# Performance work log

Measured on AMD Instinct MI355X. Metric: run time of the kernel, lower is better.

The kernel has to match this reference:

```python
import jax, jax.numpy as jnp
import numpy as np

# ---- static config (matches init_kwargs) ----
N_NODES = 100_000; N_GRAPHS = 100; NPG = 1000; GRID = 32  # ceil(sqrt(1000))
N_EDGES = 1_600_000
IN_DIM = 64; POS_DIM = 16; HID = 16; HEADS = 4; HD = HID * HEADS  # 64
OUT_DIM = 10; DIV_WEIGHT = 0.1; BN_EPS = 1e-5; NEG_SLOPE = 0.2


def _segment_softmax(e, dst, n):
    emax = jax.ops.segment_max(e, dst, num_segments=n)
    p = jnp.exp(e - emax[dst])
    denom = jax.ops.segment_sum(p, dst, num_segments=n)
    return p / (denom[dst] + 1e-16)


def _gat(x, src, dst, n, W, a_src, a_dst, extra=None):
    """GATv1-style conv: per-head linear, additive attention, segment softmax over dst."""
    H, D = a_src.shape
    h = (x @ W).reshape(n, H, D)          # [N,H,D]
    s = (h * a_src).sum(-1)               # [N,H]
    d = (h * a_dst).sum(-1)               # [N,H]
    e = s[src] + d[dst]
    if extra is not None:
        e = e + extra                     # positional attention bias [E,H]
    e = jax.nn.leaky_relu(e, NEG_SLOPE)
    alpha = _segment_softmax(e, dst, n)   # [E,H]
    out = jax.ops.segment_sum(alpha[:, :, None] * h[src], dst, num_segments=n)
    return out.reshape(n, H * D)


def _div_loss(W):
    # head-diversity / orthogonality regularizer on per-head weight slices
    in_dim = W.shape[0]
    Wh = W.reshape(in_dim, HEADS, HID).transpose(1, 0, 2).reshape(HEADS, -1)
    Wn = Wh / (jnp.linalg.norm(Wh, axis=-1, keepdims=True) + 1e-12)
    G = Wn @ Wn.T
    off = G - jnp.eye(HEADS, dtype=W.dtype)
    return DIV_WEIGHT * (off ** 2).sum() / (HEADS * (HEADS - 1))


def _grid_pos(n, dtype):
    # normalized grid positions per graph (equal-size graphs of NPG nodes)
    i = jnp.arange(n) % NPG
    return jnp.stack([(i // GRID) / (GRID - 1), (i % GRID) / (GRID - 1)], -1).astype(dtype)


def _forward(x, edge_index, batch,
             pe_W, pe_b,
             l0_pW, l0_pas, l0_pad, l0_posW, l0_posb, l0_dW, l0_das, l0_dad, l0_fW, l0_fb, l0_g, l0_b,
             l1_pW, l1_pas, l1_pad, l1_posW, l1_posb, l1_dW, l1_das, l1_dad, l1_fW, l1_fb, l1_g, l1_b,
             res_W, res_b, task_W, task_b):
    n = x.shape[0]
    src, dst = edge_index[0], edge_index[1]
    pos = _grid_pos(n, x.dtype)
    rel = pos[dst] - pos[src]             # [E,2]
    h = jnp.concatenate([x, pos @ pe_W + pe_b], -1)  # positional encoding concat [N,80]

    def layer(h_in, pW, pas, pad, posW, posb, dW, das, dad, fW, fb, g, b):
        pos_out = _gat(h_in, src, dst, n, pW, pas, pad, extra=rel @ posW + posb)
        div_out = _gat(h_in, src, dst, n, dW, das, dad)
        fused = jnp.concatenate([pos_out, div_out], -1) @ fW + fb
        mu = fused.mean(0)
        var = fused.var(0)
        bn = (fused - mu) / jnp.sqrt(var + BN_EPS) * g + b
        return jax.nn.elu(bn), _div_loss(dW)

    h1, dl0 = layer(h, l0_pW, l0_pas, l0_pad, l0_posW, l0_posb, l0_dW, l0_das, l0_dad, l0_fW, l0_fb, l0_g, l0_b)
    h2, dl1 = layer(h1, l1_pW, l1_pas, l1_pad, l1_posW, l1_posb, l1_dW, l1_das, l1_dad, l1_fW, l1_fb, l1_g, l1_b)
    h2 = h2 + (h1 @ res_W + res_b)        # residual on layer >0

    pooled = jax.ops.segment_sum(h2, batch, num_segments=N_GRAPHS) / NPG  # mean pool
    task = pooled @ task_W + task_b       # [N_GRAPHS, OUT_DIM]
    return task, dl0 + dl1


def setup_inputs() -> dict:
    key = jax.random.key(0)
    keys = iter(jax.random.split(key, 64))
    nk = lambda: next(keys)
    w = lambda shape: jax.random.normal(nk(), shape, jnp.float32) * 0.05
    x = jax.random.normal(nk(), (N_NODES, IN_DIM), jnp.float32)
    gid = jnp.repeat(jnp.arange(N_GRAPHS), N_EDGES // N_GRAPHS)
    src = gid * NPG + jax.random.randint(nk(), (N_EDGES,), 0, NPG)
    dst = gid * NPG + jax.random.randint(nk(), (N_EDGES,), 0, NPG)
    edge_index = jnp.stack([src, dst]).astype(jnp.int32)
    batch = jnp.repeat(jnp.arange(N_GRAPHS), NPG).astype(jnp.int32)
    IN0 = IN_DIM + POS_DIM
    inp = dict(x=x, edge_index=edge_index, batch=batch,
               pe_W=w((2, POS_DIM)), pe_b=jnp.zeros((POS_DIM,), jnp.float32))
    for pref, din in (('l0', IN0), ('l1', HD)):
        inp[pref + '_pW'] = w((din, HD)); inp[pref + '_pas'] = w((HEADS, HID)); inp[pref + '_pad'] = w((HEADS, HID))
        inp[pref + '_posW'] = w((2, HEADS)); inp[pref + '_posb'] = jnp.zeros((HEADS,), jnp.float32)
        inp[pref + '_dW'] = w((din, HD)); inp[pref + '_das'] = w((HEADS, HID)); inp[pref + '_dad'] = w((HEADS, HID))
        inp[pref + '_fW'] = w((2 * HD, HD)); inp[pref + '_fb'] = jnp.zeros((HD,), jnp.float32)
        inp[pref + '_g'] = jnp.ones((HD,), jnp.float32); inp[pref + '_b'] = jnp.zeros((HD,), jnp.float32)
    inp['res_W'] = w((HD, HD)); inp['res_b'] = jnp.zeros((HD,), jnp.float32)
    inp['task_W'] = w((HD, OUT_DIM)); inp['task_b'] = jnp.zeros((OUT_DIM,), jnp.float32)
    return inp


def reference(x, edge_index, batch,
              pe_W, pe_b,
              l0_pW, l0_pas, l0_pad, l0_posW, l0_posb, l0_dW, l0_das, l0_dad, l0_fW, l0_fb, l0_g, l0_b,
              l1_pW, l1_pas, l1_pad, l1_posW, l1_posb, l1_dW, l1_das, l1_dad, l1_fW, l1_fb, l1_g, l1_b,
              res_W, res_b, task_W, task_b):
    return _forward(x, edge_index, batch, pe_W, pe_b,
                    l0_pW, l0_pas, l0_pad, l0_posW, l0_posb, l0_dW, l0_das, l0_dad, l0_fW, l0_fb, l0_g, l0_b,
                    l1_pW, l1_pas, l1_pad, l1_posW, l1_posb, l1_dW, l1_das, l1_dad, l1_fW, l1_fb, l1_g, l1_b,
                    res_W, res_b, task_W, task_b)
```

## Files before the change

### kernel.cpp

```cpp
#include <hip/hip_runtime.h>
#include <math.h>

#define N_NODES   100000
#define N_GRAPHS  100
#define NPG       1000
#define N_EDGES   1600000
#define EPG       16000
#define HID       16
#define HEADS     4
#define HD        64
#define OUT_DIM   10
#define BN_EPS    1e-5f
#define NEG_SLOPE 0.2f

#define LDA 68

static const size_t OFF_PEWS  = 7000000;
static const size_t OFF_WFRAG = 7010000;
static const size_t OFF_WF2   = 7020000;
static const size_t OFF_POOL  = 7100000;
static const size_t OFF_HL    = 8000000;
static const size_t OFF_CAT   = 20800000;
static const size_t OFF_F0    = 33600000;
static const size_t OFF_F1    = 40000000;
static const size_t OFF_SPS   = 46400000;
static const size_t OFF_DPD   = 47200000;
static const size_t OFF_STATS = 48000000;
static const size_t OFF_CSR   = 48000128;
static const size_t OFF_SRT   = 48100144;

__device__ inline unsigned bf_pack(float x, float y) {
    unsigned ux = __float_as_uint(x);
    unsigned uy = __float_as_uint(y);
    ux = (ux + 0x7FFFu + ((ux >> 16) & 1u)) >> 16;
    uy = ((uy + 0x7FFFu + ((uy >> 16) & 1u)) >> 16) << 16;
    return ux | uy;
}
__device__ inline float bf_lo(unsigned u) { return __uint_as_float(u << 16); }
__device__ inline float bf_hi(unsigned u) { return __uint_as_float(u & 0xFFFF0000u); }

typedef __attribute__((ext_vector_type(8))) short bf16x8;
typedef __attribute__((ext_vector_type(4))) float f32x4;

__device__ inline bf16x8 frag_from(unsigned a, unsigned b, unsigned c, unsigned d) {
    uint4 u{a, b, c, d};
    return *reinterpret_cast<bf16x8*>(&u);
}

__global__ __launch_bounds__(1024) void sort_edges(const int* __restrict__ ei,
                                                   int* __restrict__ csr_off,
                                                   int* __restrict__ sorted_src) {
    __shared__ int hist[1024];
    __shared__ int scan[1024];
    const int g = blockIdx.x;
    const int t = threadIdx.x;
    const int* src = ei;
    const int* dst = ei + N_EDGES;
    const int e0 = g * EPG;
    const int nbase = g * NPG;

    hist[t] = 0;
    __syncthreads();
    for (int i = t; i < EPG; i += 1024) {
        int d = dst[e0 + i] - nbase;
        atomicAdd(&hist[d], 1);
    }
    __syncthreads();
    scan[t] = hist[t];
    __syncthreads();
    for (int off = 1; off < 1024; off <<= 1) {
        int v = (t >= off) ? scan[t - off] : 0;
        __syncthreads();
        scan[t] += v;
        __syncthreads();
    }
    int excl = scan[t] - hist[t];
    if (t < NPG) csr_off[nbase + t] = e0 + excl;
    if (g == 0 && t == 0) csr_off[N_NODES] = N_EDGES;
    __syncthreads();
    hist[t] = excl;
    __syncthreads();
    for (int i = t; i < EPG; i += 1024) {
        int s = src[e0 + i];
        int d = dst[e0 + i] - nbase;
        int slot = atomicAdd(&hist[d], 1);
        sorted_src[e0 + slot] = s;
    }
}

__global__ void prep_pe(const float* __restrict__ peW, const float* __restrict__ peb,
                        const float* __restrict__ Wp, const float* __restrict__ Wd,
                        float* __restrict__ pe) {
    int t = threadIdx.x;
    if (t < 128) {
        int r = t >> 6, c = t & 63;
        float sp = 0.f, sd = 0.f;
        for (int m = 0; m < 16; ++m) {
            sp += peW[r * 16 + m] * Wp[(64 + m) * 64 + c];
            sd += peW[r * 16 + m] * Wd[(64 + m) * 64 + c];
        }
        pe[r * 64 + c] = sp;
        pe[192 + r * 64 + c] = sd;
    } else if (t < 192) {
        int c = t & 63;
        float sp = 0.f, sd = 0.f;
        for (int m = 0; m < 16; ++m) {
            sp += peb[m] * Wp[(64 + m) * 64 + c];
            sd += peb[m] * Wd[(64 + m) * 64 + c];
        }
        pe[128 + c] = sp;
        pe[320 + c] = sd;
    }
}

__global__ void prep_wfrag(const float* __restrict__ fW0, const float* __restrict__ fW1,
                           uint4* __restrict__ wf) {
    const int t = threadIdx.x;
    for (int i = t; i < 2 * 4 * 4 * 64; i += 256) {
        const int lane  = i & 63;
        const int ct    = (i >> 6) & 3;
        const int kk    = (i >> 8) & 3;
        const int layer = i >> 10;
        const float* W = layer ? fW1 : fW0;
        const int col = ct * 16 + (lane & 15);
        const int kb  = kk * 32 + (lane >> 4) * 8;
        uint4 u;
        u.x = bf_pack(W[(kb + 0) * 64 + col], W[(kb + 1) * 64 + col]);
        u.y = bf_pack(W[(kb + 2) * 64 + col], W[(kb + 3) * 64 + col]);
        u.z = bf_pack(W[(kb + 4) * 64 + col], W[(kb + 5) * 64 + col]);
        u.w = bf_pack(W[(kb + 6) * 64 + col], W[(kb + 7) * 64 + col]);
        wf[i] = u;
    }
}

__global__ void prep_wfrag_dual(const float* __restrict__ pW0, const float* __restrict__ dW0,
                                const float* __restrict__ pW1, const float* __restrict__ dW1,
                                uint4* __restrict__ wf) {
    const int t = threadIdx.x;
    for (int i = t; i < 2048; i += 256) {
        const int lane  = i & 63;
        const int ct    = (i >> 6) & 3;
        const int kk    = (i >> 8) & 1;
        const int mat   = (i >> 9) & 1;
        const int layer = i >> 10;
        const float* W = layer ? (mat ? dW1 : pW1) : (mat ? dW0 : pW0);
        const int col = ct * 16 + (lane & 15);
        const int kb  = kk * 32 + (lane >> 4) * 8;
        uint4 u;
        u.x = bf_pack(W[(kb + 0) * 64 + col], W[(kb + 1) * 64 + col]);
        u.y = bf_pack(W[(kb + 2) * 64 + col], W[(kb + 3) * 64 + col]);
        u.z = bf_pack(W[(kb + 4) * 64 + col], W[(kb + 5) * 64 + col]);
        u.w = bf_pack(W[(kb + 6) * 64 + col], W[(kb + 7) * 64 + col]);
        wf[i] = u;
    }
}

template <bool PE>
__global__ __launch_bounds__(256) void gemm_dual_mfma(const float* __restrict__ A,
                                                      const unsigned* __restrict__ wf2,
                                                      const float* __restrict__ pe,
                                                      const float* __restrict__ pas,
                                                      const float* __restrict__ pad_,
                                                      const float* __restrict__ das,
                                                      const float* __restrict__ dad,
                                                      const float* __restrict__ posW,
                                                      const float* __restrict__ posb,
                                                      unsigned* __restrict__ hl,
                                                      float2* __restrict__ sps,
                                                      float2* __restrict__ dpd) {
    __shared__ float sD[4 * 2 * 16 * LDA];
    const int t = threadIdx.x;
    const int w = t >> 6, lane = t & 63;
    const int cidx = lane & 15, khi = lane >> 4;
    const int node0 = blockIdx.x * 64;

    bf16x8 wf[2][2][4];
#pragma unroll
    for (int mat = 0; mat < 2; ++mat)
#pragma unroll
        for (int kk = 0; kk < 2; ++kk)
#pragma unroll
            for (int ct = 0; ct < 4; ++ct)
                wf[mat][kk][ct] = *reinterpret_cast<const bf16x8*>(
                    wf2 + (size_t)((((mat * 2 + kk) * 4 + ct) * 64) + lane) * 4);

    int gn = node0 + w * 16 + cidx; if (gn > N_NODES - 1) gn = N_NODES - 1;
    const float* ar = A + (size_t)gn * 64;
    bf16x8 ah[2], al[2];
#pragma unroll
    for (int kk = 0; kk < 2; ++kk) {
        const int k0 = kk * 32 + khi * 8;
        float4 f0 = *reinterpret_cast<const float4*>(ar + k0);
        float4 f1 = *reinterpret_cast<const float4*>(ar + k0 + 4);
        unsigned h0 = bf_pack(f0.x, f0.y), h1 = bf_pack(f0.z, f0.w);
        unsigned h2 = bf_pack(f1.x, f1.y), h3 = bf_pack(f1.z, f1.w);
        unsigned l0 = bf_pack(f0.x - bf_lo(h0), f0.y - bf_hi(h0));
        unsigned l1 = bf_pack(f0.z - bf_lo(h1), f0.w - bf_hi(h1));
        unsigned l2 = bf_pack(f1.x - bf_lo(h2), f1.y - bf_hi(h2));
        unsigned l3 = bf_pack(f1.z - bf_lo(h3), f1.w - bf_hi(h3));
        ah[kk] = frag_from(h0, h1, h2, h3);
        al[kk] = frag_from(l0, l1, l2, l3);
    }

    f32x4 ap[4], ad[4];
#pragma unroll
    for (int ct = 0; ct < 4; ++ct) { ap[ct] = 0.f; ad[ct] = 0.f; }
#pragma unroll
    for (int ct = 0; ct < 4; ++ct) {
        ap[ct] = __builtin_amdgcn_mfma_f32_16x16x32_bf16(ah[0], wf[0][0][ct], ap[ct], 0, 0, 0);
        ap[ct] = __builtin_amdgcn_mfma_f32_16x16x32_bf16(ah[1], wf[0][1][ct], ap[ct], 0, 0, 0);
        ap[ct] = __builtin_amdgcn_mfma_f32_16x16x32_bf16(al[0], wf[0][0][ct], ap[ct], 0, 0, 0);
        ap[ct] = __builtin_amdgcn_mfma_f32_16x16x32_bf16(al[1], wf[0][1][ct], ap[ct], 0, 0, 0);
        ad[ct] = __builtin_amdgcn_mfma_f32_16x16x32_bf16(ah[0], wf[1][0][ct], ad[ct], 0, 0, 0);
        ad[ct] = __builtin_amdgcn_mfma_f32_16x16x32_bf16(ah[1], wf[1][1][ct], ad[ct], 0, 0, 0);
        ad[ct] = __builtin_amdgcn_mfma_f32_16x16x32_bf16(al[0], wf[1][0][ct], ad[ct], 0, 0, 0);
        ad[ct] = __builtin_amdgcn_mfma_f32_16x16x32_bf16(al[1], wf[1][1][ct], ad[ct], 0, 0, 0);
    }

    {
        float* base = sD + w * (2 * 16 * LDA);
#pragma unroll
        for (int ct = 0; ct < 4; ++ct)
#pragma unroll
            for (int q = 0; q < 4; ++q) {
                base[(khi * 4 + q) * LDA + ct * 16 + cidx]                 = ap[ct][q];
                base[16 * LDA + (khi * 4 + q) * LDA + ct * 16 + cidx]      = ad[ct][q];
            }
    }
    __syncthreads();

    const int tx = t & 15, ty = t >> 4;
    const int c4 = tx * 4;
    float4 accp[4], accd[4];
#pragma unroll
    for (int j = 0; j < 4; ++j) {
        const int n = ty * 4 + j;
        const float* bp = sD + (n >> 4) * (2 * 16 * LDA) + (n & 15) * LDA;
        accp[j] = *reinterpret_cast<const float4*>(bp + c4);
        accd[j] = *reinterpret_cast<const float4*>(bp + 16 * LDA + c4);
    }

    if (PE) {
        float4 pp0 = *reinterpret_cast<const float4*>(&pe[c4]);
        float4 pp1 = *reinterpret_cast<const float4*>(&pe[64 + c4]);
        float4 ppb = *reinterpret_cast<const float4*>(&pe[128 + c4]);
        float4 pd0 = *reinterpret_cast<const float4*>(&pe[192 + c4]);
        float4 pd1 = *reinterpret_cast<const float4*>(&pe[256 + c4]);
        float4 pdb = *reinterpret_cast<const float4*>(&pe[320 + c4]);
#pragma unroll
        for (int j = 0; j < 4; ++j) {
            int node = node0 + ty * 4 + j;
            int r = node % NPG;
            float px = (float)(r >> 5) * (1.0f / 31.0f);
            float py = (float)(r & 31) * (1.0f / 31.0f);
            accp[j].x += px * pp0.x + py * pp1.x + ppb.x;
            accp[j].y += px * pp0.y + py * pp1.y + ppb.y;
            accp[j].z += px * pp0.z + py * pp1.z + ppb.z;
            accp[j].w += px * pp0.w + py * pp1.w + ppb.w;
            accd[j].x += px * pd0.x + py * pd1.x + pdb.x;
            accd[j].y += px * pd0.y + py * pd1.y + pdb.y;
            accd[j].z += px * pd0.z + py * pd1.z + pdb.z;
            accd[j].w += px * pd0.w + py * pd1.w + pdb.w;
        }
    }

    float4 pasv = *reinterpret_cast<const float4*>(&pas[c4]);
    float4 padv = *reinterpret_cast<const float4*>(&pad_[c4]);
    float4 dasv = *reinterpret_cast<const float4*>(&das[c4]);
    float4 dadv = *reinterpret_cast<const float4*>(&dad[c4]);
    const int h = tx >> 2;
    const float pw0 = posW[h], pw1 = posW[4 + h], pb = posb[h];
    const int cu = tx * 2;
#pragma unroll
    for (int j = 0; j < 4; ++j) {
        const int node = node0 + ty * 4 + j;
        float vps = accp[j].x * pasv.x + accp[j].y * pasv.y + accp[j].z * pasv.z + accp[j].w * pasv.w;
        float vpd = accp[j].x * padv.x + accp[j].y * padv.y + accp[j].z * padv.z + accp[j].w * padv.w;
        float vds = accd[j].x * dasv.x + accd[j].y * dasv.y + accd[j].z * dasv.z + accd[j].w * dasv.w;
        float vdd = accd[j].x * dadv.x + accd[j].y * dadv.y + accd[j].z * dadv.z + accd[j].w * dadv.w;
        vps += __shfl_xor(vps, 1); vps += __shfl_xor(vps, 2);
        vpd += __shfl_xor(vpd, 1); vpd += __shfl_xor(vpd, 2);
        vds += __shfl_xor(vds, 1); vds += __shfl_xor(vds, 2);
        vdd += __shfl_xor(vdd, 1); vdd += __shfl_xor(vdd, 2);
        if (node < N_NODES) {
            uint2 up, ud;
            up.x = bf_pack(accp[j].x, accp[j].y); up.y = bf_pack(accp[j].z, accp[j].w);
            ud.x = bf_pack(accd[j].x, accd[j].y); ud.y = bf_pack(accd[j].z, accd[j].w);
            *reinterpret_cast<uint2*>(&hl[(size_t)node * 64 + cu])      = up;
            *reinterpret_cast<uint2*>(&hl[(size_t)node * 64 + 32 + cu]) = ud;
            if ((tx & 3) == 0) {
                const int r = node % NPG;
                const float pxn = (float)(r >> 5) * (1.0f / 31.0f);
                const float pyn = (float)(r & 31) * (1.0f / 31.0f);
                const float posdot = pxn * pw0 + pyn * pw1;
                sps[node * 4 + h] = float2{vps - posdot, vds};
                dpd[node * 4 + h] = float2{vpd + posdot + pb, vdd};
            }
        }
    }
}

__global__ __launch_bounds__(256) void gemm_mfma_bf(const unsigned* __restrict__ A,
                                                    const unsigned* __restrict__ wfrag,
                                                    const float* __restrict__ bias,
                                                    float* __restrict__ out,
                                                    float* __restrict__ stats) {
    __shared__ float red[512];
    const int t = threadIdx.x;
    const int lane = t & 63;
    const int cidx = lane & 15;
    const int khi  = lane >> 4;

    bf16x8 wf[4][4];
#pragma unroll
    for (int kk = 0; kk < 4; ++kk)
#pragma unroll
        for (int ct = 0; ct < 4; ++ct)
            wf[kk][ct] = *reinterpret_cast<const bf16x8*>(wfrag + (size_t)((kk * 4 + ct) * 64 + lane) * 4);

    float bias_r[4];
#pragma unroll
    for (int ct = 0; ct < 4; ++ct) bias_r[ct] = bias[ct * 16 + cidx];

    float ls[4] = {0.f, 0.f, 0.f, 0.f};
    float lq[4] = {0.f, 0.f, 0.f, 0.f};

    const int NW  = gridDim.x << 2;
    const int wid = (blockIdx.x << 2) + (t >> 6);
    for (int tile = wid; tile < N_NODES / 16; tile += NW) {
        const int node0 = tile << 4;
        const unsigned* arow = A + (size_t)(node0 + cidx) * 64 + khi * 4;
        bf16x8 a0 = *reinterpret_cast<const bf16x8*>(arow);
        bf16x8 a1 = *reinterpret_cast<const bf16x8*>(arow + 16);
        bf16x8 a2 = *reinterpret_cast<const bf16x8*>(arow + 32);
        bf16x8 a3 = *reinterpret_cast<const bf16x8*>(arow + 48);

        f32x4 acc[4];
#pragma unroll
        for (int ct = 0; ct < 4; ++ct) acc[ct] = 0.f;
#pragma unroll
        for (int ct = 0; ct < 4; ++ct) {
            acc[ct] = __builtin_amdgcn_mfma_f32_16x16x32_bf16(a0, wf[0][ct], acc[ct], 0, 0, 0);
            acc[ct] = __builtin_amdgcn_mfma_f32_16x16x32_bf16(a1, wf[1][ct], acc[ct], 0, 0, 0);
            acc[ct] = __builtin_amdgcn_mfma_f32_16x16x32_bf16(a2, wf[2][ct], acc[ct], 0, 0, 0);
            acc[ct] = __builtin_amdgcn_mfma_f32_16x16x32_bf16(a3, wf[3][ct], acc[ct], 0, 0, 0);
        }

        const int nbase = node0 + (khi << 2);
#pragma unroll
        for (int ct = 0; ct < 4; ++ct) {
#pragma unroll
            for (int q = 0; q < 4; ++q) {
                float v = acc[ct][q] + bias_r[ct];
                out[(size_t)(nbase + q) * 64 + ct * 16 + cidx] = v;
                ls[ct] += v;
                lq[ct] = fmaf(v, v, lq[ct]);
            }
        }
    }

#pragma unroll
    for (int ct = 0; ct < 4; ++ct) {
        ls[ct] += __shfl_xor(ls[ct], 16); ls[ct] += __shfl_xor(ls[ct], 32);
        lq[ct] += __shfl_xor(lq[ct], 16); lq[ct] += __shfl_xor(lq[ct], 32);
    }
    if (lane < 16) {
        const int w = t >> 6;
#pragma unroll
        for (int ct = 0; ct < 4; ++ct) {
            red[w * 64 + ct * 16 + lane]       = ls[ct];
            red[256 + w * 64 + ct * 16 + lane] = lq[ct];
        }
    }
    __syncthreads();
    if (t < 64) {
        float s  = red[t] + red[64 + t] + red[128 + t] + red[192 + t];
        float sq = red[256 + t] + red[320 + t] + red[384 + t] + red[448 + t];
        atomicAdd(&stats[t], s);
        atomicAdd(&stats[64 + t], sq);
    }
}

__global__ __launch_bounds__(256) void gat_fused(const unsigned* __restrict__ hl,
                                                 const float2* __restrict__ sps,
                                                 const float2* __restrict__ dpd,
                                                 const int* __restrict__ csr_off,
                                                 const int* __restrict__ sorted_src,
                                                 unsigned* __restrict__ gat_cat) {
    const int b = blockIdx.x;
    const int logical = (b & 7) * 3125 + (b >> 3);
    const int v = logical * 4 + (threadIdx.x >> 6);
    if (v >= N_NODES) return;
    const int lane = threadIdx.x & 63;
    const int j1 = lane >> 3;
    const int p1 = (lane >> 2) & 1;
    const int h1 = lane & 3;
    const int phneed = ((lane >> 5) << 2) | ((lane & 31) >> 3);

    const float2 dv1 = dpd[(size_t)v * 4 + h1];
    const float dval1 = p1 ? dv1.y : dv1.x;

    const int beg = __builtin_amdgcn_readfirstlane(csr_off[v]);
    const int end = __builtin_amdgcn_readfirstlane(csr_off[v + 1]);

    float2 acc = {0.f, 0.f};
    float wpart = 0.f;
    int e = beg;
    for (; e + 8 <= end; e += 8) {
        int s = sorted_src[e + j1];
        float2 sv = sps[(size_t)s * 4 + h1];
        float elog = (p1 ? sv.y : sv.x) + dval1;
        elog = fmaxf(elog, NEG_SLOPE * elog);
        float w = __expf(elog);
        wpart += w;
#pragma unroll
        for (int jj = 0; jj < 8; ++jj) {
            int sj = __builtin_amdgcn_readlane(s, jj * 8);
            float wj = __shfl(w, jj * 8 + phneed);
            unsigned u = hl[((size_t)sj << 6) + lane];
            acc.x = fmaf(wj, bf_lo(u), acc.x);
            acc.y = fmaf(wj, bf_hi(u), acc.y);
        }
    }
    if (e < end) {
        const int nj = end - e;
        int ee = e + j1; if (ee >= end) ee = end - 1;
        int s = sorted_src[ee];
        float2 sv = sps[(size_t)s * 4 + h1];
        float elog = (p1 ? sv.y : sv.x) + dval1;
        elog = fmaxf(elog, NEG_SLOPE * elog);
        float w = __expf(elog);
        if (j1 >= nj) w = 0.f;
        wpart += w;
        for (int jj = 0; jj < nj; ++jj) {
            int sj = __builtin_amdgcn_readlane(s, jj * 8);
            float wj = __shfl(w, jj * 8 + phneed);
            unsigned u = hl[((size_t)sj << 6) + lane];
            acc.x = fmaf(wj, bf_lo(u), acc.x);
            acc.y = fmaf(wj, bf_hi(u), acc.y);
        }
    }
    wpart += __shfl_xor(wpart, 8);
    wpart += __shfl_xor(wpart, 16);
    wpart += __shfl_xor(wpart, 32);
    const float wsum = __shfl(wpart, phneed);
    const float inv = 1.0f / (wsum + 1e-16f);
    gat_cat[(size_t)v * 64 + lane] = bf_pack(acc.x * inv, acc.y * inv);
}

template <bool WRITEF>
__global__ __launch_bounds__(256) void bn_elu(float* __restrict__ F, const float* __restrict__ stats,
                                              const float* __restrict__ gamma, const float* __restrict__ beta,
                                              float* __restrict__ pooled) {
    __shared__ float red[256];
    const int t = threadIdx.x;
    const int idx = blockIdx.x * 256 + t;
    const int c = t & 63;
    float mu = stats[c] * (1.0f / (float)N_NODES);
    float var = stats[64 + c] * (1.0f / (float)N_NODES) - mu * mu;
    float inv = rsqrtf(var + BN_EPS);
    float v = (F[idx] - mu) * inv * gamma[c] + beta[c];
    v = (v > 0.f) ? v : expm1f(v);
    if (WRITEF) F[idx] = v;
    red[t] = v;
    __syncthreads();
    if (t < 64) {
        float s = red[c] + red[64 + c] + red[128 + c] + red[192 + c];
        int g = (blockIdx.x * 4) / NPG;
        atomicAdd(&pooled[g * 64 + c], s);
    }
}

__global__ __launch_bounds__(64) void task_head(const float* __restrict__ pooled,
                                                const float* __restrict__ pooledF0,
                                                const float* __restrict__ resW,
                                                const float* __restrict__ resb,
                                                const float* __restrict__ taskW,
                                                const float* __restrict__ taskb,
                                                float* __restrict__ out) {
    const int g = blockIdx.x;
    const int c = threadIdx.x;
    float rc = 0.f;
    const float* pf = pooledF0 + g * 64;
    for (int k = 0; k < 64; ++k)
        rc = fmaf(pf[k], resW[k * 64 + c], rc);
    float p = (pooled[g * 64 + c] + rc) * (1.0f / (float)NPG) + resb[c];
#pragma unroll
    for (int o = 0; o < OUT_DIM; ++o) {
        float partial = p * taskW[c * OUT_DIM + o];
#pragma unroll
        for (int m = 1; m < 64; m <<= 1) partial += __shfl_xor(partial, m);
        if (c == 0) out[g * OUT_DIM + o] = partial + taskb[o];
    }
}

__global__ __launch_bounds__(256) void div_loss(const float* __restrict__ dW0,
                                                const float* __restrict__ dW1,
                                                float* __restrict__ out) {
    __shared__ float red[16][16];
    float total = 0.f;
    for (int layer = 0; layer < 2; ++layer) {
        const float* W = layer ? dW1 : dW0;
        const int din = layer ? 64 : 80;
        const int p = threadIdx.x & 15;
        const int s16 = threadIdx.x >> 4;
        const int i = p >> 2, j = p & 3;
        float acc = 0.f;
        const int Kk = din * 16;
        for (int kk = s16; kk < Kk; kk += 16) {
            int rrow = kk >> 4, cc = kk & 15;
            acc += W[rrow * 64 + i * 16 + cc] * W[rrow * 64 + j * 16 + cc];
        }
        red[p][s16] = acc;
        __syncthreads();
        if (threadIdx.x < 16) {
            float s = 0.f;
            for (int m = 0; m < 16; ++m) s += red[threadIdx.x][m];
            red[threadIdx.x][0] = s;
        }
        __syncthreads();
        if (threadIdx.x == 0) {
            float G[4][4], nrm[4];
            for (int a = 0; a < 4; ++a)
                for (int b = 0; b < 4; ++b) G[a][b] = red[a * 4 + b][0];
            for (int a = 0; a < 4; ++a) nrm[a] = sqrtf(G[a][a]) + 1e-12f;
            float l = 0.f;
            for (int a = 0; a < 4; ++a)
                for (int b = 0; b < 4; ++b) {
                    float gn = G[a][b] / (nrm[a] * nrm[b]);
                    float off = gn - (a == b ? 1.f : 0.f);
                    l += off * off;
                }
            total += 0.1f * l / 12.f;
        }
        __syncthreads();
    }
    if (threadIdx.x == 0) *out = total;
}

extern "C" void kernel_launch(void* const* d_in, const int* in_sizes, int n_in,
                              void* d_out, int out_size, void* d_ws, size_t ws_size,
                              hipStream_t stream) {
    const float* x      = (const float*)d_in[0];
    const int*   ei     = (const int*)d_in[1];
    const float* peW    = (const float*)d_in[3];
    const float* peb    = (const float*)d_in[4];

    const float* l_pW[2]   = {(const float*)d_in[5],  (const float*)d_in[17]};
    const float* l_pas[2]  = {(const float*)d_in[6],  (const float*)d_in[18]};
    const float* l_pad[2]  = {(const float*)d_in[7],  (const float*)d_in[19]};
    const float* l_posW[2] = {(const float*)d_in[8],  (const float*)d_in[20]};
    const float* l_posb[2] = {(const float*)d_in[9],  (const float*)d_in[21]};
    const float* l_dW[2]   = {(const float*)d_in[10], (const float*)d_in[22]};
    const float* l_das[2]  = {(const float*)d_in[11], (const float*)d_in[23]};
    const float* l_dad[2]  = {(const float*)d_in[12], (const float*)d_in[24]};
    const float* l_fW[2]   = {(const float*)d_in[13], (const float*)d_in[25]};
    const float* l_fb[2]   = {(const float*)d_in[14], (const float*)d_in[26]};
    const float* l_g[2]    = {(const float*)d_in[15], (const float*)d_in[27]};
    const float* l_b[2]    = {(const float*)d_in[16], (const float*)d_in[28]};
    const float* res_W  = (const float*)d_in[29];
    const float* res_b  = (const float*)d_in[30];
    const float* task_W = (const float*)d_in[31];
    const float* task_b = (const float*)d_in[32];

    float* ws = (float*)d_ws;
    float* pe_ws   = ws + OFF_PEWS;
    float* wfrag   = ws + OFF_WFRAG;
    float* wfrag2  = ws + OFF_WF2;
    float* pooled  = ws + OFF_POOL;
    float* pooledF0= ws + OFF_POOL + 6400;
    unsigned* hl   = (unsigned*)(ws + OFF_HL);
    unsigned* cat_bf = (unsigned*)(ws + OFF_CAT);
    float* F0      = ws + OFF_F0;
    float* F1      = ws + OFF_F1;
    float2* sps    = (float2*)(ws + OFF_SPS);
    float2* dpd    = (float2*)(ws + OFF_DPD);
    float* stats   = ws + OFF_STATS;
    int*   csr_off    = (int*)(ws + OFF_CSR);
    int*   sorted_src = (int*)(ws + OFF_SRT);
    float* out = (float*)d_out;

    const int NODE_BLOCKS = (N_NODES + 3) / 4;
    const int GEMM_BLOCKS = (N_NODES + 63) / 64;
    const int MFMA_BLOCKS = 1563;
    const int BN_BLOCKS   = N_NODES * 64 / 256;

    sort_edges<<<N_GRAPHS, 1024, 0, stream>>>(ei, csr_off, sorted_src);
    prep_pe<<<1, 256, 0, stream>>>(peW, peb, l_pW[0], l_dW[0], pe_ws);
    prep_wfrag<<<1, 256, 0, stream>>>(l_fW[0], l_fW[1], (uint4*)wfrag);
    prep_wfrag_dual<<<1, 256, 0, stream>>>(l_pW[0], l_dW[0], l_pW[1], l_dW[1], (uint4*)wfrag2);
    hipMemsetAsync(pooled, 0, 2 * N_GRAPHS * 64 * sizeof(float), stream);

    gemm_dual_mfma<true><<<GEMM_BLOCKS, 256, 0, stream>>>(x, (const unsigned*)wfrag2, pe_ws,
        l_pas[0], l_pad[0], l_das[0], l_dad[0], l_posW[0], l_posb[0],
        hl, sps, dpd);
    gat_fused<<<NODE_BLOCKS, 256, 0, stream>>>(hl, sps, dpd, csr_off, sorted_src, cat_bf);
    hipMemsetAsync(stats, 0, 128 * sizeof(float), stream);
    gemm_mfma_bf<<<MFMA_BLOCKS, 256, 0, stream>>>(cat_bf, (const unsigned*)wfrag,
                                                  l_fb[0], F0, stats);
    bn_elu<true><<<BN_BLOCKS, 256, 0, stream>>>(F0, stats, l_g[0], l_b[0], pooledF0);

    gemm_dual_mfma<false><<<GEMM_BLOCKS, 256, 0, stream>>>(F0, (const unsigned*)wfrag2 + 4096, pe_ws,
        l_pas[1], l_pad[1], l_das[1], l_dad[1], l_posW[1], l_posb[1],
        hl, sps, dpd);
    gat_fused<<<NODE_BLOCKS, 256, 0, stream>>>(hl, sps, dpd, csr_off, sorted_src, cat_bf);
    hipMemsetAsync(stats, 0, 128 * sizeof(float), stream);
    gemm_mfma_bf<<<MFMA_BLOCKS, 256, 0, stream>>>(cat_bf, (const unsigned*)wfrag + 4096,
                                                  l_fb[1], F1, stats);
    bn_elu<false><<<BN_BLOCKS, 256, 0, stream>>>(F1, stats, l_g[1], l_b[1], pooled);

    task_head<<<N_GRAPHS, 64, 0, stream>>>(pooled, pooledF0, res_W, res_b,
                                           task_W, task_b, out);
    div_loss<<<1, 256, 0, stream>>>(l_dW[0], l_dW[1], out + 1000);
}
```

Measured before the change: 483.1 us.

## Fuse layer-0 BN+ELU into layer-1 GEMM, merge prep kernels, prefetch GAT sources

Removes the layer-0 bn_elu pass by applying batch-norm scale/shift and ELU while loading F0 inside the layer-1 dual GEMM, which also does the per-graph pooling with wave shuffles and atomics. The three prep kernels and the memsets are merged into one 4-block prep_all launch, and the two layers now use separate stats buffers. The source-score array is split into two planar float arrays, and the GAT edge loop software-pipelines the sorted_src and score loads two iterations ahead. The cost is extra per-element BN/ELU arithmetic and atomics in the GEMM, plus more registers held in the GAT loop.

After: 496.3 us. 2.7% more time.

```diff
diff --git a/kernel.cpp b/kernel.cpp
--- a/kernel.cpp
+++ b/kernel.cpp
@@ -16,6 +16,7 @@
 #define LDA 68
 
 static const size_t OFF_PEWS  = 7000000;
+static const size_t OFF_STAT1 = 7001000;
 static const size_t OFF_WFRAG = 7010000;
 static const size_t OFF_WF2   = 7020000;
 static const size_t OFF_POOL  = 7100000;
@@ -23,7 +24,8 @@
 static const size_t OFF_CAT   = 20800000;
 static const size_t OFF_F0    = 33600000;
 static const size_t OFF_F1    = 40000000;
-static const size_t OFF_SPS   = 46400000;
+static const size_t OFF_SPSP  = 46400000;
+static const size_t OFF_SPSD  = 46800000;
 static const size_t OFF_DPD   = 47200000;
 static const size_t OFF_STATS = 48000000;
 static const size_t OFF_CSR   = 48000128;
@@ -88,74 +90,78 @@
     }
 }
 
-__global__ void prep_pe(const float* __restrict__ peW, const float* __restrict__ peb,
-                        const float* __restrict__ Wp, const float* __restrict__ Wd,
-                        float* __restrict__ pe) {
-    int t = threadIdx.x;
-    if (t < 128) {
-        int r = t >> 6, c = t & 63;
-        float sp = 0.f, sd = 0.f;
-        for (int m = 0; m < 16; ++m) {
-            sp += peW[r * 16 + m] * Wp[(64 + m) * 64 + c];
-            sd += peW[r * 16 + m] * Wd[(64 + m) * 64 + c];
-        }
-        pe[r * 64 + c] = sp;
-        pe[192 + r * 64 + c] = sd;
-    } else if (t < 192) {
-        int c = t & 63;
-        float sp = 0.f, sd = 0.f;
-        for (int m = 0; m < 16; ++m) {
-            sp += peb[m] * Wp[(64 + m) * 64 + c];
-            sd += peb[m] * Wd[(64 + m) * 64 + c];
-        }
-        pe[128 + c] = sp;
-        pe[320 + c] = sd;
-    }
-}
-
-__global__ void prep_wfrag(const float* __restrict__ fW0, const float* __restrict__ fW1,
-                           uint4* __restrict__ wf) {
+__global__ __launch_bounds__(256) void prep_all(const float* __restrict__ peW, const float* __restrict__ peb,
+                                                const float* __restrict__ pW0, const float* __restrict__ dW0,
+                                                const float* __restrict__ pW1, const float* __restrict__ dW1,
+                                                const float* __restrict__ fW0, const float* __restrict__ fW1,
+                                                float* __restrict__ pe,
+                                                uint4* __restrict__ wfA,
+                                                uint4* __restrict__ wfD,
+                                                float* __restrict__ pool2,
+                                                float* __restrict__ stats0,
+                                                float* __restrict__ stats1) {
     const int t = threadIdx.x;
-    for (int i = t; i < 2 * 4 * 4 * 64; i += 256) {
-        const int lane  = i & 63;
-        const int ct    = (i >> 6) & 3;
-        const int kk    = (i >> 8) & 3;
-        const int layer = i >> 10;
-        const float* W = layer ? fW1 : fW0;
-        const int col = ct * 16 + (lane & 15);
-        const int kb  = kk * 32 + (lane >> 4) * 8;
-        uint4 u;
-        u.x = bf_pack(W[(kb + 0) * 64 + col], W[(kb + 1) * 64 + col]);
-        u.y = bf_pack(W[(kb + 2) * 64 + col], W[(kb + 3) * 64 + col]);
-        u.z = bf_pack(W[(kb + 4) * 64 + col], W[(kb + 5) * 64 + col]);
-        u.w = bf_pack(W[(kb + 6) * 64 + col], W[(kb + 7) * 64 + col]);
-        wf[i] = u;
-    }
-}
-
-__global__ void prep_wfrag_dual(const float* __restrict__ pW0, const float* __restrict__ dW0,
-                                const float* __restrict__ pW1, const float* __restrict__ dW1,
-                                uint4* __restrict__ wf) {
-    const int t = threadIdx.x;
-    for (int i = t; i < 2048; i += 256) {
-        const int lane  = i & 63;
-        const int ct    = (i >> 6) & 3;
-        const int kk    = (i >> 8) & 1;
-        const int mat   = (i >> 9) & 1;
-        const int layer = i >> 10;
-        const float* W = layer ? (mat ? dW1 : pW1) : (mat ? dW0 : pW0);
-        const int col = ct * 16 + (lane & 15);
-        const int kb  = kk * 32 + (lane >> 4) * 8;
-        uint4 u;
-        u.x = bf_pack(W[(kb + 0) * 64 + col], W[(kb + 1) * 64 + col]);
-        u.y = bf_pack(W[(kb + 2) * 64 + col], W[(kb + 3) * 64 + col]);
-        u.z = bf_pack(W[(kb + 4) * 64 + col], W[(kb + 5) * 64 + col]);
-        u.w = bf_pack(W[(kb + 6) * 64 + col], W[(kb + 7) * 64 + col]);
-        wf[i] = u;
-    }
-}
-
-template <bool PE>
+    const int b = blockIdx.x;
+    if (b == 0) {
+        if (t < 128) {
+            int r = t >> 6, c = t & 63;
+            float sp = 0.f, sd = 0.f;
+            for (int m = 0; m < 16; ++m) {
+                sp += peW[r * 16 + m] * pW0[(64 + m) * 64 + c];
+                sd += peW[r * 16 + m] * dW0[(64 + m) * 64 + c];
+            }
+            pe[r * 64 + c] = sp;
+            pe[192 + r * 64 + c] = sd;
+        } else if (t < 192) {
+            int c = t & 63;
+            float sp = 0.f, sd = 0.f;
+            for (int m = 0; m < 16; ++m) {
+                sp += peb[m] * pW0[(64 + m) * 64 + c];
+                sd += peb[m] * dW0[(64 + m) * 64 + c];
+            }
+            pe[128 + c] = sp;
+            pe[320 + c] = sd;
+        }
+    } else if (b == 1) {
+        for (int i = t; i < 2 * 4 * 4 * 64; i += 256) {
+            const int lane  = i & 63;
+            const int ct    = (i >> 6) & 3;
+            const int kk    = (i >> 8) & 3;
+            const int layer = i >> 10;
+            const float* W = layer ? fW1 : fW0;
+            const int col = ct * 16 + (lane & 15);
+            const int kb  = kk * 32 + (lane >> 4) * 8;
+            uint4 u;
+            u.x = bf_pack(W[(kb + 0) * 64 + col], W[(kb + 1) * 64 + col]);
+            u.y = bf_pack(W[(kb + 2) * 64 + col], W[(kb + 3) * 64 + col]);
+            u.z = bf_pack(W[(kb + 4) * 64 + col], W[(kb + 5) * 64 + col]);
+            u.w = bf_pack(W[(kb + 6) * 64 + col], W[(kb + 7) * 64 + col]);
+            wfA[i] = u;
+        }
+    } else if (b == 2) {
+        for (int i = t; i < 2048; i += 256) {
+            const int lane  = i & 63;
+            const int ct    = (i >> 6) & 3;
+            const int kk    = (i >> 8) & 1;
+            const int mat   = (i >> 9) & 1;
+            const int layer = i >> 10;
+            const float* W = layer ? (mat ? dW1 : pW1) : (mat ? dW0 : pW0);
+            const int col = ct * 16 + (lane & 15);
+            const int kb  = kk * 32 + (lane >> 4) * 8;
+            uint4 u;
+            u.x = bf_pack(W[(kb + 0) * 64 + col], W[(kb + 1) * 64 + col]);
+            u.y = bf_pack(W[(kb + 2) * 64 + col], W[(kb + 3) * 64 + col]);
+            u.z = bf_pack(W[(kb + 4) * 64 + col], W[(kb + 5) * 64 + col]);
+            u.w = bf_pack(W[(kb + 6) * 64 + col], W[(kb + 7) * 64 + col]);
+            wfD[i] = u;
+        }
+    } else {
+        for (int i = t; i < 2 * N_GRAPHS * 64; i += 256) pool2[i] = 0.f;
+        if (t < 128) { stats0[t] = 0.f; stats1[t] = 0.f; }
+    }
+}
+
+template <bool PE, bool BN>
 __global__ __launch_bounds__(256) void gemm_dual_mfma(const float* __restrict__ A,
                                                       const unsigned* __restrict__ wf2,
                                                       const float* __restrict__ pe,
@@ -165,8 +171,13 @@
                                                       const float* __restrict__ dad,
                                                       const float* __restrict__ posW,
                                                       const float* __restrict__ posb,
+                                                      const float* __restrict__ stats,
+                                                      const float* __restrict__ gamma,
+                                                      const float* __restrict__ beta,
+                                                      float* __restrict__ poolF,
                                                       unsigned* __restrict__ hl,
-                                                      float2* __restrict__ sps,
+                                                      float* __restrict__ sps_p,
+                                                      float* __restrict__ sps_d,
                                                       float2* __restrict__ dpd) {
     __shared__ float sD[4 * 2 * 16 * LDA];
     const int t = threadIdx.x;
@@ -184,7 +195,8 @@
                 wf[mat][kk][ct] = *reinterpret_cast<const bf16x8*>(
                     wf2 + (size_t)((((mat * 2 + kk) * 4 + ct) * 64) + lane) * 4);
 
-    int gn = node0 + w * 16 + cidx; if (gn > N_NODES - 1) gn = N_NODES - 1;
+    const int node0w = node0 + w * 16;
+    int gn = node0w + cidx; if (gn > N_NODES - 1) gn = N_NODES - 1;
     const float* ar = A + (size_t)gn * 64;
     bf16x8 ah[2], al[2];
 #pragma unroll
@@ -192,6 +204,65 @@
         const int k0 = kk * 32 + khi * 8;
         float4 f0 = *reinterpret_cast<const float4*>(ar + k0);
         float4 f1 = *reinterpret_cast<const float4*>(ar + k0 + 4);
+        if (BN) {
+            const float invN = 1.0f / (float)N_NODES;
+            float4 sa = *reinterpret_cast<const float4*>(&stats[k0]);
+            float4 sb = *reinterpret_cast<const float4*>(&stats[k0 + 4]);
+            float4 qa = *reinterpret_cast<const float4*>(&stats[64 + k0]);
+            float4 qb = *reinterpret_cast<const float4*>(&stats[64 + k0 + 4]);
+            float4 ga = *reinterpret_cast<const float4*>(&gamma[k0]);
+            float4 gb = *reinterpret_cast<const float4*>(&gamma[k0 + 4]);
+            float4 ba = *reinterpret_cast<const float4*>(&beta[k0]);
+            float4 bb = *reinterpret_cast<const float4*>(&beta[k0 + 4]);
+            float sc[8], sh[8];
+            float ss[8] = {sa.x, sa.y, sa.z, sa.w, sb.x, sb.y, sb.z, sb.w};
+            float qq[8] = {qa.x, qa.y, qa.z, qa.w, qb.x, qb.y, qb.z, qb.w};
+            float gg[8] = {ga.x, ga.y, ga.z, ga.w, gb.x, gb.y, gb.z, gb.w};
+            float bt[8] = {ba.x, ba.y, ba.z, ba.w, bb.x, bb.y, bb.z, bb.w};
+#pragma unroll
+            for (int i = 0; i < 8; ++i) {
+                float mu = ss[i] * invN;
+                float var = qq[i] * invN - mu * mu;
+                float iv = rsqrtf(var + BN_EPS);
+                sc[i] = iv * gg[i];
+                sh[i] = bt[i] - mu * sc[i];
+            }
+            auto ap = [&](float v, int i) {
+                float r = fmaf(v, sc[i], sh[i]);
+                return r > 0.f ? r : (__expf(r) - 1.f);
+            };
+            f0.x = ap(f0.x, 0); f0.y = ap(f0.y, 1); f0.z = ap(f0.z, 2); f0.w = ap(f0.w, 3);
+            f1.x = ap(f1.x, 4); f1.y = ap(f1.y, 5); f1.z = ap(f1.z, 6); f1.w = ap(f1.w, 7);
+            if (node0w < N_NODES) {
+                const int node_l = node0w + cidx;
+                const bool okn = node_l < N_NODES;
+                const int gl = node_l / NPG;
+                const int g0 = node0w / NPG;
+                int lastn = node0w + 15; if (lastn > N_NODES - 1) lastn = N_NODES - 1;
+                const int g1 = lastn / NPG;
+                float p8[8] = {f0.x, f0.y, f0.z, f0.w, f1.x, f1.y, f1.z, f1.w};
+                {
+                    const bool m = okn && (gl == g0);
+#pragma unroll
+                    for (int i = 0; i < 8; ++i) {
+                        float tv = m ? p8[i] : 0.f;
+                        tv += __shfl_xor(tv, 1); tv += __shfl_xor(tv, 2);
+                        tv += __shfl_xor(tv, 4); tv += __shfl_xor(tv, 8);
+                        if (cidx == 0) atomicAdd(&poolF[g0 * 64 + k0 + i], tv);
+                    }
+                }
+                if (g1 != g0) {
+                    const bool m = okn && (gl == g1);
+#pragma unroll
+                    for (int i = 0; i < 8; ++i) {
+                        float tv = m ? p8[i] : 0.f;
+                        tv += __shfl_xor(tv, 1); tv += __shfl_xor(tv, 2);
+                        tv += __shfl_xor(tv, 4); tv += __shfl_xor(tv, 8);
+                        if (cidx == 0) atomicAdd(&poolF[g1 * 64 + k0 + i], tv);
+                    }
+                }
+            }
+        }
         unsigned h0 = bf_pack(f0.x, f0.y), h1 = bf_pack(f0.z, f0.w);
         unsigned h2 = bf_pack(f1.x, f1.y), h3 = bf_pack(f1.z, f1.w);
         unsigned l0 = bf_pack(f0.x - bf_lo(h0), f0.y - bf_hi(h0));
@@ -202,19 +273,19 @@
         al[kk] = frag_from(l0, l1, l2, l3);
     }
 
-    f32x4 ap[4], ad[4];
-#pragma unroll
-    for (int ct = 0; ct < 4; ++ct) { ap[ct] = 0.f; ad[ct] = 0.f; }
+    f32x4 ap4[4], ad4[4];
+#pragma unroll
+    for (int ct = 0; ct < 4; ++ct) { ap4[ct] = 0.f; ad4[ct] = 0.f; }
 #pragma unroll
     for (int ct = 0; ct < 4; ++ct) {
-        ap[ct] = __builtin_amdgcn_mfma_f32_16x16x32_bf16(ah[0], wf[0][0][ct], ap[ct], 0, 0, 0);
-        ap[ct] = __builtin_amdgcn_mfma_f32_16x16x32_bf16(ah[1], wf[0][1][ct], ap[ct], 0, 0, 0);
-        ap[ct] = __builtin_amdgcn_mfma_f32_16x16x32_bf16(al[0], wf[0][0][ct], ap[ct], 0, 0, 0);
-        ap[ct] = __builtin_amdgcn_mfma_f32_16x16x32_bf16(al[1], wf[0][1][ct], ap[ct], 0, 0, 0);
-        ad[ct] = __builtin_amdgcn_mfma_f32_16x16x32_bf16(ah[0], wf[1][0][ct], ad[ct], 0, 0, 0);
-        ad[ct] = __builtin_amdgcn_mfma_f32_16x16x32_bf16(ah[1], wf[1][1][ct], ad[ct], 0, 0, 0);
-        ad[ct] = __builtin_amdgcn_mfma_f32_16x16x32_bf16(al[0], wf[1][0][ct], ad[ct], 0, 0, 0);
-        ad[ct] = __builtin_amdgcn_mfma_f32_16x16x32_bf16(al[1], wf[1][1][ct], ad[ct], 0, 0, 0);
+        ap4[ct] = __builtin_amdgcn_mfma_f32_16x16x32_bf16(ah[0], wf[0][0][ct], ap4[ct], 0, 0, 0);
+        ap4[ct] = __builtin_amdgcn_mfma_f32_16x16x32_bf16(ah[1], wf[0][1][ct], ap4[ct], 0, 0, 0);
+        ap4[ct] = __builtin_amdgcn_mfma_f32_16x16x32_bf16(al[0], wf[0][0][ct], ap4[ct], 0, 0, 0);
+        ap4[ct] = __builtin_amdgcn_mfma_f32_16x16x32_bf16(al[1], wf[0][1][ct], ap4[ct], 0, 0, 0);
+        ad4[ct] = __builtin_amdgcn_mfma_f32_16x16x32_bf16(ah[0], wf[1][0][ct], ad4[ct], 0, 0, 0);
+        ad4[ct] = __builtin_amdgcn_mfma_f32_16x16x32_bf16(ah[1], wf[1][1][ct], ad4[ct], 0, 0, 0);
+        ad4[ct] = __builtin_amdgcn_mfma_f32_16x16x32_bf16(al[0], wf[1][0][ct], ad4[ct], 0, 0, 0);
+        ad4[ct] = __builtin_amdgcn_mfma_f32_16x16x32_bf16(al[1], wf[1][1][ct], ad4[ct], 0, 0, 0);
     }
 
     {
@@ -223,8 +294,8 @@
         for (int ct = 0; ct < 4; ++ct)
 #pragma unroll
             for (int q = 0; q < 4; ++q) {
-                base[(khi * 4 + q) * LDA + ct * 16 + cidx]                 = ap[ct][q];
-                base[16 * LDA + (khi * 4 + q) * LDA + ct * 16 + cidx]      = ad[ct][q];
+                base[(khi * 4 + q) * LDA + ct * 16 + cidx]                 = ap4[ct][q];
+                base[16 * LDA + (khi * 4 + q) * LDA + ct * 16 + cidx]      = ad4[ct][q];
             }
     }
     __syncthreads();
@@ -293,7 +364,8 @@
                 const float pxn = (float)(r >> 5) * (1.0f / 31.0f);
                 const float pyn = (float)(r & 31) * (1.0f / 31.0f);
                 const float posdot = pxn * pw0 + pyn * pw1;
-                sps[node * 4 + h] = float2{vps - posdot, vds};
+                sps_p[node * 4 + h] = vps - posdot;
+                sps_d[node * 4 + h] = vds;
                 dpd[node * 4 + h] = float2{vpd + posdot + pb, vdd};
             }
         }
@@ -382,7 +454,8 @@
 }
 
 __global__ __launch_bounds__(256) void gat_fused(const unsigned* __restrict__ hl,
-                                                 const float2* __restrict__ sps,
+                                                 const float* __restrict__ sps_p,
+                                                 const float* __restrict__ sps_d,
                                                  const float2* __restrict__ dpd,
                                                  const int* __restrict__ csr_off,
                                                  const int* __restrict__ sorted_src,
@@ -397,6 +470,7 @@
     const int h1 = lane & 3;
     const int phneed = ((lane >> 5) << 2) | ((lane & 31) >> 3);
 
+    const float* __restrict__ spl = p1 ? sps_d : sps_p;
     const float2 dv1 = dpd[(size_t)v * 4 + h1];
     const float dval1 = p1 ? dv1.y : dv1.x;
 
@@ -406,28 +480,38 @@
     float2 acc = {0.f, 0.f};
     float wpart = 0.f;
     int e = beg;
-    for (; e + 8 <= end; e += 8) {
-        int s = sorted_src[e + j1];
-        float2 sv = sps[(size_t)s * 4 + h1];
-        float elog = (p1 ? sv.y : sv.x) + dval1;
+    const int nfull = (end - beg) >> 3;
+
+    int sA = 0, sB = 0;
+    float svA = 0.f, svB = 0.f;
+    if (nfull >= 1) { sA = sorted_src[e + j1]; svA = spl[(size_t)sA * 4 + h1]; }
+    if (nfull >= 2) { sB = sorted_src[e + 8 + j1]; }
+
+    for (int k = 0; k < nfull; ++k, e += 8) {
+        int sC = 0;
+        if (k + 2 < nfull) sC = sorted_src[e + 16 + j1];
+        if (k + 1 < nfull) svB = spl[(size_t)sB * 4 + h1];
+        float elog = svA + dval1;
         elog = fmaxf(elog, NEG_SLOPE * elog);
         float w = __expf(elog);
         wpart += w;
 #pragma unroll
         for (int jj = 0; jj < 8; ++jj) {
-            int sj = __builtin_amdgcn_readlane(s, jj * 8);
+            int sj = __builtin_amdgcn_readlane(sA, jj * 8);
             float wj = __shfl(w, jj * 8 + phneed);
             unsigned u = hl[((size_t)sj << 6) + lane];
             acc.x = fmaf(wj, bf_lo(u), acc.x);
             acc.y = fmaf(wj, bf_hi(u), acc.y);
         }
-    }
+        sA = sB; sB = sC; svA = svB;
+    }
+
     if (e < end) {
         const int nj = end - e;
         int ee = e + j1; if (ee >= end) ee = end - 1;
         int s = sorted_src[ee];
-        float2 sv = sps[(size_t)s * 4 + h1];
-        float elog = (p1 ? sv.y : sv.x) + dval1;
+        float sval = spl[(size_t)s * 4 + h1];
+        float elog = sval + dval1;
         elog = fmaxf(elog, NEG_SLOPE * elog);
         float w = __expf(elog);
         if (j1 >= nj) w = 0.f;
@@ -565,6 +649,7 @@
 
     float* ws = (float*)d_ws;
     float* pe_ws   = ws + OFF_PEWS;
+    float* stats1  = ws + OFF_STAT1;
     float* wfrag   = ws + OFF_WFRAG;
     float* wfrag2  = ws + OFF_WF2;
     float* pooled  = ws + OFF_POOL;
@@ -573,9 +658,10 @@
     unsigned* cat_bf = (unsigned*)(ws + OFF_CAT);
     float* F0      = ws + OFF_F0;
     float* F1      = ws + OFF_F1;
-    float2* sps    = (float2*)(ws + OFF_SPS);
+    float* sps_p   = ws + OFF_SPSP;
+    float* sps_d   = ws + OFF_SPSD;
     float2* dpd    = (float2*)(ws + OFF_DPD);
-    float* stats   = ws + OFF_STATS;
+    float* stats0  = ws + OFF_STATS;
     int*   csr_off    = (int*)(ws + OFF_CSR);
     int*   sorted_src = (int*)(ws + OFF_SRT);
     float* out = (float*)d_out;
@@ -586,28 +672,27 @@
     const int BN_BLOCKS   = N_NODES * 64 / 256;
 
     sort_edges<<<N_GRAPHS, 1024, 0, stream>>>(ei, csr_off, sorted_src);
-    prep_pe<<<1, 256, 0, stream>>>(peW, peb, l_pW[0], l_dW[0], pe_ws);
-    prep_wfrag<<<1, 256, 0, stream>>>(l_fW[0], l_fW[1], (uint4*)wfrag);
-    prep_wfrag_dual<<<1, 256, 0, stream>>>(l_pW[0], l_dW[0], l_pW[1], l_dW[1], (uint4*)wfrag2);
-    hipMemsetAsync(pooled, 0, 2 * N_GRAPHS * 64 * sizeof(float), stream);
-
-    gemm_dual_mfma<true><<<GEMM_BLOCKS, 256, 0, stream>>>(x, (const unsigned*)wfrag2, pe_ws,
+    prep_all<<<4, 256, 0, stream>>>(peW, peb, l_pW[0], l_dW[0], l_pW[1], l_dW[1],
+                                    l_fW[0], l_fW[1], pe_ws,
+                                    (uint4*)wfrag, (uint4*)wfrag2,
+                                    pooled, stats0, stats1);
+
+    gemm_dual_mfma<true, false><<<GEMM_BLOCKS, 256, 0, stream>>>(x, (const unsigned*)wfrag2, pe_ws,
         l_pas[0], l_pad[0], l_das[0], l_dad[0], l_posW[0], l_posb[0],
-        hl, sps, dpd);
-    gat_fused<<<NODE_BLOCKS, 256, 0, stream>>>(hl, sps, dpd, csr_off, sorted_src, cat_bf);
-    hipMemsetAsync(stats, 0, 128 * sizeof(float), stream);
+        stats0, l_g[0], l_b[0], pooledF0,
+        hl, sps_p, sps_d, dpd);
+    gat_fused<<<NODE_BLOCKS, 256, 0, stream>>>(hl, sps_p, sps_d, dpd, csr_off, sorted_src, cat_bf);
     gemm_mfma_bf<<<MFMA_BLOCKS, 256, 0, stream>>>(cat_bf, (const unsigned*)wfrag,
-                                                  l_fb[0], F0, stats);
-    bn_elu<true><<<BN_BLOCKS, 256, 0, stream>>>(F0, stats, l_g[0], l_b[0], pooledF0);
-
-    gemm_dual_mfma<false><<<GEMM_BLOCKS, 256, 0, stream>>>(F0, (const unsigned*)wfrag2 + 4096, pe_ws,
+                                                  l_fb[0], F0, stats0);
+
+    gemm_dual_mfma<false, true><<<GEMM_BLOCKS, 256, 0, stream>>>(F0, (const unsigned*)wfrag2 + 4096, pe_ws,
         l_pas[1], l_pad[1], l_das[1], l_dad[1], l_posW[1], l_posb[1],
-        hl, sps, dpd);
-    gat_fused<<<NODE_BLOCKS, 256, 0, stream>>>(hl, sps, dpd, csr_off, sorted_src, cat_bf);
-    hipMemsetAsync(stats, 0, 128 * sizeof(float), stream);
+        stats0, l_g[0], l_b[0], pooledF0,
+        hl, sps_p, sps_d, dpd);
+    gat_fused<<<NODE_BLOCKS, 256, 0, stream>>>(hl, sps_p, sps_d, dpd, csr_off, sorted_src, cat_bf);
     gemm_mfma_bf<<<MFMA_BLOCKS, 256, 0, stream>>>(cat_bf, (const unsigned*)wfrag + 4096,
-                                                  l_fb[1], F1, stats);
-    bn_elu<false><<<BN_BLOCKS, 256, 0, stream>>>(F1, stats, l_g[1], l_b[1], pooled);
+                                                  l_fb[1], F1, stats1);
+    bn_elu<false><<<BN_BLOCKS, 256, 0, stream>>>(F1, stats1, l_g[1], l_b[1], pooled);
 
     task_head<<<N_GRAPHS, 64, 0, stream>>>(pooled, pooledF0, res_W, res_b,
                                            task_W, task_b, out);
```
